# Kernel tuning notes

Measured on AMD Instinct MI355X. Metric: run time of the kernel, lower is better.

## Reference

```python
import jax, jax.numpy as jnp
import numpy as np

B, S, D, H = 2, 2048, 1024, 16
DK = D // H


def setup_inputs() -> dict:
    key = jax.random.key(0)
    ks = jax.random.split(key, 12)
    scale = 1.0 / np.sqrt(D)
    inp = {
        "Q": jax.random.normal(ks[0], (B, S, D), jnp.float32),
        "K": jax.random.normal(ks[1], (B, S, D), jnp.float32),
        "V": jax.random.normal(ks[2], (B, S, D), jnp.float32),
        # causal mask, broadcastable to [B, H, S, S]; 0 -> masked
        "Mask": jnp.tril(jnp.ones((S, S), jnp.int32))[None, None],
        "Wq": jax.random.normal(ks[3], (D, D), jnp.float32) * scale,
        "bq": jnp.zeros((D,), jnp.float32),
        "Wk": jax.random.normal(ks[4], (D, D), jnp.float32) * scale,
        "bk": jnp.zeros((D,), jnp.float32),
        "Wv": jax.random.normal(ks[5], (D, D), jnp.float32) * scale,
        "bv": jnp.zeros((D,), jnp.float32),
        "Wo": jax.random.normal(ks[6], (D, D), jnp.float32) * scale,
        "bo": jnp.zeros((D,), jnp.float32),
    }
    return inp


def _heads(x):
    # [B, S, D] -> [B, H, S, DK]
    return x.reshape(B, S, H, DK).transpose(0, 2, 1, 3)


def reference(Q, K, V, Mask, Wq, bq, Wk, bk, Wv, bv, Wo, bo):
    q = _heads(Q @ Wq.T + bq)
    k = _heads(K @ Wk.T + bk)
    v = _heads(V @ Wv.T + bv)
    # NOTE: original module does NOT scale by 1/sqrt(d_k)
    logits = jnp.einsum("bhqd,bhkd->bhqk", q, k)
    logits = jnp.where(Mask == 0, jnp.float32(-1e9), logits)
    attn = jax.nn.softmax(logits, axis=-1)  # dropout p=0.0 -> identity
    ctx = jnp.einsum("bhqk,bhkd->bhqd", attn, v)
    ctx = ctx.transpose(0, 2, 1, 3).reshape(B, S, D)
    return ctx @ Wo.T + bo
```

## Files before the change

### kernel.cpp

```cpp
#include <hip/hip_runtime.h>
#include <hip/hip_bf16.h>

#define B_  2
#define S_  2048
#define D_  1024
#define H_  16
#define DK_ 64
#define M_  (B_ * S_)

typedef __bf16 bf16;
typedef __bf16 bf16x8 __attribute__((ext_vector_type(8)));
typedef __bf16 bf16x4 __attribute__((ext_vector_type(4)));
typedef float  f32x4  __attribute__((ext_vector_type(4)));

#define MFMA16(a, b, c) __builtin_amdgcn_mfma_f32_16x16x32_bf16((a), (b), (c), 0, 0, 0)

__device__ __forceinline__ void gl2lds16(const bf16* g, bf16* l) {
    __builtin_amdgcn_global_load_lds((const __attribute__((address_space(1))) void*)g,
                                     (__attribute__((address_space(3))) void*)l, 16, 0, 0);
}

struct CastArgs { const float* src[7]; bf16* dst[7]; };

__global__ __launch_bounds__(256) void cast_all(CastArgs a) {
    int i = blockIdx.x * 256 + threadIdx.x;
    int seg, off;
    if (i < 3145728) { seg = i >> 20; off = i & 1048575; }
    else { int j = i - 3145728; seg = 3 + (j >> 18); off = j & 262143; }
    float4 v = ((const float4*)a.src[seg])[off];
    bf16x4 o;
    o[0] = (bf16)v.x; o[1] = (bf16)v.y; o[2] = (bf16)v.z; o[3] = (bf16)v.w;
    *(bf16x4*)&a.dst[seg][(size_t)off * 4] = o;
}

struct QkvArgs { const bf16* A[3]; const bf16* W[3]; const float* bias[3]; bf16* out[3]; };

__global__ __launch_bounds__(256, 3) void gemm_qkv(QkvArgs ar) {
    __shared__ char smem[34816];
    bf16* As = (bf16*)smem;
    bf16* Bs = (bf16*)(smem + 16384);
    bf16* Cs = (bf16*)smem;

    const int hid = (blockIdx.z * gridDim.y + blockIdx.y) * gridDim.x + blockIdx.x;
    const int swz = (hid & 7) * 96 + (hid >> 3);
    const int bx = swz & 7, by = (swz >> 3) & 31, z = swz >> 8;

    const bf16* A  = ar.A[z];
    const bf16* Bt = ar.W[z];
    const float* bias = ar.bias[z];
    bf16* Out = ar.out[z];
    const int mode = (z == 2) ? 1 : 0;

    const int t = threadIdx.x, lane = t & 63, w = t >> 6;
    const int lr = lane & 15, lq = lane >> 4;
    const int wm = (w >> 1) * 64, wn = (w & 1) * 64;
    const int n0 = bx * 128, m0 = by * 128;

    const bf16* Ag[4]; const bf16* Bg[4]; bf16* Al[4]; bf16* Bl[4];
#pragma unroll
    for (int i = 0; i < 4; ++i) {
        int c = i * 256 + w * 64 + lane;
        int row = c >> 3, x = (c & 7) ^ (row & 7);
        Ag[i] = A  + (size_t)(m0 + row) * 1024 + x * 8;
        Bg[i] = Bt + (size_t)(n0 + row) * 1024 + x * 8;
        Al[i] = As + (i * 256 + w * 64) * 8;
        Bl[i] = Bs + (i * 256 + w * 64) * 8;
    }

    f32x4 acc[4][4];
#pragma unroll
    for (int mi = 0; mi < 4; ++mi)
#pragma unroll
        for (int ni = 0; ni < 4; ++ni) acc[mi][ni] = 0.0f;

    for (int k0 = 0; k0 < 1024; k0 += 64) {
        __syncthreads();
#pragma unroll
        for (int i = 0; i < 4; ++i) {
            gl2lds16(Ag[i] + k0, Al[i]);
            gl2lds16(Bg[i] + k0, Bl[i]);
        }
        __syncthreads();
#pragma unroll
        for (int ks = 0; ks < 2; ++ks) {
            bf16x8 af[4], bfr[4];
#pragma unroll
            for (int mi = 0; mi < 4; ++mi) {
                int row = wm + mi * 16 + lr;
                af[mi] = *(const bf16x8*)&As[row * 64 + ((ks * 4 + lq) ^ (row & 7)) * 8];
            }
#pragma unroll
            for (int ni = 0; ni < 4; ++ni) {
                int row = wn + ni * 16 + lr;
                bfr[ni] = *(const bf16x8*)&Bs[row * 64 + ((ks * 4 + lq) ^ (row & 7)) * 8];
            }
#pragma unroll
            for (int mi = 0; mi < 4; ++mi)
#pragma unroll
                for (int ni = 0; ni < 4; ++ni) acc[mi][ni] = MFMA16(af[mi], bfr[ni], acc[mi][ni]);
        }
    }

    if (mode == 0) {
#pragma unroll
        for (int mi = 0; mi < 4; ++mi) {
#pragma unroll
            for (int ni = 0; ni < 4; ++ni) {
                int gn = n0 + wn + ni * 16 + lr;
                float bv = bias[gn];
#pragma unroll
                for (int r = 0; r < 4; ++r) {
                    int gm = m0 + wm + mi * 16 + lq * 4 + r;
                    float v = acc[mi][ni][r] + bv;
                    int b = gm >> 11, s = gm & (S_ - 1);
                    int h = gn >> 6, dk = gn & 63;
                    Out[(((size_t)(b * H_ + h) * S_ + s) << 6) + dk] = (bf16)v;
                }
            }
        }
    } else {
        __syncthreads();
#pragma unroll
        for (int mi = 0; mi < 4; ++mi) {
#pragma unroll
            for (int ni = 0; ni < 4; ++ni) {
                int n = wn + ni * 16 + lr;
                float bv = bias[n0 + n];
                bf16x4 pk;
#pragma unroll
                for (int r = 0; r < 4; ++r) pk[r] = (bf16)(acc[mi][ni][r] + bv);
                *(bf16x4*)&Cs[n * 136 + wm + mi * 16 + lq * 4] = pk;
            }
        }
        __syncthreads();
        const int b = m0 >> 11, s0 = m0 & (S_ - 1);
#pragma unroll
        for (int j = 0; j < 8; ++j) {
            int cc = j * 256 + t;
            int n = cc >> 4, cm = cc & 15;
            int gn = n0 + n, h = gn >> 6, dk = gn & 63;
            bf16x8 v = *(const bf16x8*)&Cs[n * 136 + cm * 8];
            *(bf16x8*)&Out[(((size_t)(b * H_ + h) * DK_ + dk) << 11) + s0 + cm * 8] = v;
        }
    }
}

__global__ __launch_bounds__(256, 2) void gemm_out(const bf16* __restrict__ A,
                                                   const bf16* __restrict__ Bt,
                                                   const float* __restrict__ bias,
                                                   float* __restrict__ Out) {
    __shared__ bf16 As[64 * 64];
    __shared__ bf16 Bs[128 * 64];

    const int hid = blockIdx.y * gridDim.x + blockIdx.x;
    const int swz = (hid & 7) * 64 + (hid >> 3);
    const int bx = swz & 7, by = swz >> 3;

    const int t = threadIdx.x, lane = t & 63, w = t >> 6;
    const int lr = lane & 15, lq = lane >> 4;
    const int wm = (w >> 1) * 32, wn = (w & 1) * 64;
    const int n0 = bx * 128, m0 = by * 64;

    const bf16* Ag[2]; bf16* Al[2];
#pragma unroll
    for (int i = 0; i < 2; ++i) {
        int c = i * 256 + w * 64 + lane;
        int row = c >> 3, x = (c & 7) ^ (row & 7);
        Ag[i] = A + (size_t)(m0 + row) * 1024 + x * 8;
        Al[i] = As + (i * 256 + w * 64) * 8;
    }
    const bf16* Bg[4]; bf16* Bl[4];
#pragma unroll
    for (int i = 0; i < 4; ++i) {
        int c = i * 256 + w * 64 + lane;
        int row = c >> 3, x = (c & 7) ^ (row & 7);
        Bg[i] = Bt + (size_t)(n0 + row) * 1024 + x * 8;
        Bl[i] = Bs + (i * 256 + w * 64) * 8;
    }

    f32x4 acc[2][4];
#pragma unroll
    for (int mi = 0; mi < 2; ++mi)
#pragma unroll
        for (int ni = 0; ni < 4; ++ni) acc[mi][ni] = 0.0f;

    for (int k0 = 0; k0 < 1024; k0 += 64) {
        __syncthreads();
#pragma unroll
        for (int i = 0; i < 2; ++i) gl2lds16(Ag[i] + k0, Al[i]);
#pragma unroll
        for (int i = 0; i < 4; ++i) gl2lds16(Bg[i] + k0, Bl[i]);
        __syncthreads();
#pragma unroll
        for (int ks = 0; ks < 2; ++ks) {
            bf16x8 af[2], bfr[4];
#pragma unroll
            for (int mi = 0; mi < 2; ++mi) {
                int row = wm + mi * 16 + lr;
                af[mi] = *(const bf16x8*)&As[row * 64 + ((ks * 4 + lq) ^ (row & 7)) * 8];
            }
#pragma unroll
            for (int ni = 0; ni < 4; ++ni) {
                int row = wn + ni * 16 + lr;
                bfr[ni] = *(const bf16x8*)&Bs[row * 64 + ((ks * 4 + lq) ^ (row & 7)) * 8];
            }
#pragma unroll
            for (int mi = 0; mi < 2; ++mi)
#pragma unroll
                for (int ni = 0; ni < 4; ++ni) acc[mi][ni] = MFMA16(af[mi], bfr[ni], acc[mi][ni]);
        }
    }

#pragma unroll
    for (int mi = 0; mi < 2; ++mi) {
#pragma unroll
        for (int ni = 0; ni < 4; ++ni) {
            int gn = n0 + wn + ni * 16 + lr;
            float bv = bias[gn];
#pragma unroll
            for (int r = 0; r < 4; ++r) {
                int gm = m0 + wm + mi * 16 + lq * 4 + r;
                Out[(size_t)gm * 1024 + gn] = acc[mi][ni][r] + bv;
            }
        }
    }
}

__global__ __launch_bounds__(256, 2) void flash_attn(const bf16* __restrict__ qh,
                                                     const bf16* __restrict__ kh,
                                                     const bf16* __restrict__ vt,
                                                     bf16* __restrict__ ctx) {
    __shared__ char smem[33280];
    bf16* Ks = (bf16*)smem;
    bf16* Ps = (bf16*)(smem + 16384);
    float* Op = (float*)(smem + 16384);
    float* Lh = (float*)(smem + 32768);

    const int id = blockIdx.x;
    const int xcd = id & 7, loc = id >> 3;
    const int bh = xcd * 4 + (loc & 3);
    const int pair = loc >> 2;
    const int b = bh >> 4, h = bh & 15;

    const bf16* Qp = qh + (size_t)bh * S_ * DK_;
    const bf16* Kp = kh + (size_t)bh * S_ * DK_;
    const bf16* Vp = vt + (size_t)bh * DK_ * S_;

    const int t = threadIdx.x, lane = t & 63, w = t >> 6;
    const int lr = lane & 15, lq = lane >> 4;
    const int wq = w & 1, wk = w >> 1;
    bf16* Pw = Ps + w * 2048;

    for (int half = 0; half < 2; ++half) {
        const int qt = half ? (31 - pair) : pair;

        bf16x8 qreg[2][2];
#pragma unroll
        for (int ks = 0; ks < 2; ++ks)
#pragma unroll
            for (int nt = 0; nt < 2; ++nt)
                qreg[ks][nt] = *(const bf16x8*)(Qp +
                    (size_t)(qt * 64 + wq * 32 + nt * 16 + lr) * 64 + ks * 32 + lq * 8);

        f32x4 oacc[2][4];
#pragma unroll
        for (int mt = 0; mt < 2; ++mt)
#pragma unroll
            for (int nt = 0; nt < 4; ++nt) oacc[mt][nt] = 0.0f;
        float lpart[2] = {0.f, 0.f};

        const int nkt = qt / 2 + 1;
        for (int kt = 0; kt < nkt; ++kt) {
            __syncthreads();
#pragma unroll
            for (int i = 0; i < 4; ++i) {
                int c = w * 256 + i * 64 + lane;
                int krow = c >> 3, xx = (c & 7) ^ (krow & 7);
                gl2lds16(Kp + (size_t)(kt * 128 + krow) * 64 + xx * 8, Ks + (w * 256 + i * 64) * 8);
            }
            __syncthreads();

            const int k64 = kt * 2 + wk;
            if (k64 <= qt) {
                bf16x8 bv[2][4];
#pragma unroll
                for (int kk = 0; kk < 2; ++kk)
#pragma unroll
                    for (int nt = 0; nt < 4; ++nt)
                        bv[kk][nt] = *(const bf16x8*)(Vp + (size_t)(nt * 16 + lr) * S_ +
                                                      kt * 128 + wk * 64 + kk * 32 + lq * 8);
                f32x4 s[4][2];
#pragma unroll
                for (int mt = 0; mt < 4; ++mt)
#pragma unroll
                    for (int nt = 0; nt < 2; ++nt) s[mt][nt] = 0.0f;
#pragma unroll
                for (int ks = 0; ks < 2; ++ks) {
                    bf16x8 af[4];
                    int xx = (ks * 4 + lq) ^ (lr & 7);
#pragma unroll
                    for (int mt = 0; mt < 4; ++mt)
                        af[mt] = *(const bf16x8*)&Ks[(wk * 64 + mt * 16 + lr) * 64 + xx * 8];
#pragma unroll
                    for (int mt = 0; mt < 4; ++mt)
#pragma unroll
                        for (int nt = 0; nt < 2; ++nt) s[mt][nt] = MFMA16(af[mt], qreg[ks][nt], s[mt][nt]);
                }
                const bool diag = (k64 == qt);
#pragma unroll
                for (int mt = 0; mt < 4; ++mt)
#pragma unroll
                    for (int nt = 0; nt < 2; ++nt) {
                        bf16x4 pb;
#pragma unroll
                        for (int r = 0; r < 4; ++r) {
                            int kl = mt * 16 + lq * 4 + r;
                            int qlT = wq * 32 + nt * 16 + lr;
                            float p = (!diag || kl <= qlT) ? __expf(s[mt][nt][r]) : 0.0f;
                            bf16 p16 = (bf16)p;
                            lpart[nt] += (float)p16;
                            pb[r] = p16;
                        }
                        int xx = (2 * mt + (lq >> 1)) ^ (lr & 7);
                        *(bf16x4*)&Pw[(nt * 16 + lr) * 64 + xx * 8 + (lq & 1) * 4] = pb;
                    }
#pragma unroll
                for (int kk = 0; kk < 2; ++kk) {
                    bf16x8 ap[2];
                    int xx = (kk * 4 + lq) ^ (lr & 7);
#pragma unroll
                    for (int mt2 = 0; mt2 < 2; ++mt2)
                        ap[mt2] = *(const bf16x8*)&Pw[(mt2 * 16 + lr) * 64 + xx * 8];
#pragma unroll
                    for (int mt2 = 0; mt2 < 2; ++mt2)
#pragma unroll
                        for (int nt = 0; nt < 4; ++nt)
                            oacc[mt2][nt] = MFMA16(ap[mt2], bv[kk][nt], oacc[mt2][nt]);
                }
            }
        }

        __syncthreads();
#pragma unroll
        for (int nt = 0; nt < 2; ++nt) {
            lpart[nt] += __shfl_xor(lpart[nt], 16);
            lpart[nt] += __shfl_xor(lpart[nt], 32);
        }
        if (lq == 0)
#pragma unroll
            for (int nt = 0; nt < 2; ++nt) Lh[wk * 64 + wq * 32 + nt * 16 + lr] = lpart[nt];
        if (wk == 1) {
#pragma unroll
            for (int mt = 0; mt < 2; ++mt)
#pragma unroll
                for (int nt = 0; nt < 4; ++nt)
#pragma unroll
                    for (int r = 0; r < 4; ++r) {
                        int row = mt * 16 + lq * 4 + r, col = nt * 16 + lr;
                        int xx = (col >> 2) ^ (row & 15);
                        Op[wq * 2048 + row * 64 + xx * 4 + (col & 3)] = oacc[mt][nt][r];
                    }
        }
        __syncthreads();
        if (wk == 0) {
            float linv[2][4];
#pragma unroll
            for (int mt = 0; mt < 2; ++mt)
#pragma unroll
                for (int r = 0; r < 4; ++r) {
                    int qq = wq * 32 + mt * 16 + lq * 4 + r;
                    linv[mt][r] = 1.0f / (Lh[qq] + Lh[64 + qq]);
                }
#pragma unroll
            for (int mt = 0; mt < 2; ++mt)
#pragma unroll
                for (int nt = 0; nt < 4; ++nt)
#pragma unroll
                    for (int r = 0; r < 4; ++r) {
                        int row = mt * 16 + lq * 4 + r, col = nt * 16 + lr;
                        int xx = (col >> 2) ^ (row & 15);
                        float v = (oacc[mt][nt][r] + Op[wq * 2048 + row * 64 + xx * 4 + (col & 3)]) * linv[mt][r];
                        int q = qt * 64 + wq * 32 + row;
                        ctx[((size_t)(b * S_ + q)) * D_ + h * DK_ + col] = (bf16)v;
                    }
        }
        __syncthreads();
    }
}

extern "C" void kernel_launch(void* const* d_in, const int* in_sizes, int n_in,
                              void* d_out, int out_size, void* d_ws, size_t ws_size,
                              hipStream_t stream) {
    const float* Q  = (const float*)d_in[0];
    const float* K  = (const float*)d_in[1];
    const float* V  = (const float*)d_in[2];
    const float* Wq = (const float*)d_in[4];
    const float* bq = (const float*)d_in[5];
    const float* Wk = (const float*)d_in[6];
    const float* bk = (const float*)d_in[7];
    const float* Wv = (const float*)d_in[8];
    const float* bv = (const float*)d_in[9];
    const float* Wo = (const float*)d_in[10];
    const float* bo = (const float*)d_in[11];

    char* p = (char*)d_ws;
    bf16* Qb  = (bf16*)p;  p += (size_t)M_ * D_ * 2;
    bf16* Kb  = (bf16*)p;  p += (size_t)M_ * D_ * 2;
    bf16* Vb  = (bf16*)p;  p += (size_t)M_ * D_ * 2;
    bf16* Wqb = (bf16*)p;  p += (size_t)D_ * D_ * 2;
    bf16* Wkb = (bf16*)p;  p += (size_t)D_ * D_ * 2;
    bf16* Wvb = (bf16*)p;  p += (size_t)D_ * D_ * 2;
    bf16* Wob = (bf16*)p;  p += (size_t)D_ * D_ * 2;
    bf16* qhd = (bf16*)p;  p += (size_t)M_ * D_ * 2;
    bf16* khd = (bf16*)p;  p += (size_t)M_ * D_ * 2;
    bf16* vtr = (bf16*)p;  p += (size_t)M_ * D_ * 2;
    bf16* ctx = (bf16*)p;  p += (size_t)M_ * D_ * 2;

    CastArgs ca;
    ca.src[0] = Q;  ca.dst[0] = Qb;
    ca.src[1] = K;  ca.dst[1] = Kb;
    ca.src[2] = V;  ca.dst[2] = Vb;
    ca.src[3] = Wq; ca.dst[3] = Wqb;
    ca.src[4] = Wk; ca.dst[4] = Wkb;
    ca.src[5] = Wv; ca.dst[5] = Wvb;
    ca.src[6] = Wo; ca.dst[6] = Wob;
    cast_all<<<16384, 256, 0, stream>>>(ca);

    QkvArgs qa;
    qa.A[0] = Qb;  qa.A[1] = Kb;  qa.A[2] = Vb;
    qa.W[0] = Wqb; qa.W[1] = Wkb; qa.W[2] = Wvb;
    qa.bias[0] = bq; qa.bias[1] = bk; qa.bias[2] = bv;
    qa.out[0] = qhd; qa.out[1] = khd; qa.out[2] = vtr;
    dim3 qgrid(D_ / 128, M_ / 128, 3);
    gemm_qkv<<<qgrid, 256, 0, stream>>>(qa);

    flash_attn<<<512, 256, 0, stream>>>(qhd, khd, vtr, ctx);

    dim3 ogrid(D_ / 128, M_ / 64);
    gemm_out<<<ogrid, 256, 0, stream>>>(ctx, Wob, bo, (float*)d_out);
}
```

Measured before the change: 213.8 us.

## Stage QKV epilogue through LDS, grid-stride cast kernel, raise MFMA wave priority

```diff
diff --git a/kernel.cpp b/kernel.cpp
--- a/kernel.cpp
+++ b/kernel.cpp
@@ -23,14 +23,15 @@
 struct CastArgs { const float* src[7]; bf16* dst[7]; };
 
 __global__ __launch_bounds__(256) void cast_all(CastArgs a) {
-    int i = blockIdx.x * 256 + threadIdx.x;
-    int seg, off;
-    if (i < 3145728) { seg = i >> 20; off = i & 1048575; }
-    else { int j = i - 3145728; seg = 3 + (j >> 18); off = j & 262143; }
-    float4 v = ((const float4*)a.src[seg])[off];
-    bf16x4 o;
-    o[0] = (bf16)v.x; o[1] = (bf16)v.y; o[2] = (bf16)v.z; o[3] = (bf16)v.w;
-    *(bf16x4*)&a.dst[seg][(size_t)off * 4] = o;
+    for (int i = blockIdx.x * 256 + threadIdx.x; i < 4194304; i += 2048 * 256) {
+        int seg, off;
+        if (i < 3145728) { seg = i >> 20; off = i & 1048575; }
+        else { int j = i - 3145728; seg = 3 + (j >> 18); off = j & 262143; }
+        float4 v = ((const float4*)a.src[seg])[off];
+        bf16x4 o;
+        o[0] = (bf16)v.x; o[1] = (bf16)v.y; o[2] = (bf16)v.z; o[3] = (bf16)v.w;
+        *(bf16x4*)&a.dst[seg][(size_t)off * 4] = o;
+    }
 }
 
 struct QkvArgs { const bf16* A[3]; const bf16* W[3]; const float* bias[3]; bf16* out[3]; };
@@ -102,21 +103,28 @@
     }
 
     if (mode == 0) {
+        __syncthreads();
 #pragma unroll
         for (int mi = 0; mi < 4; ++mi) {
 #pragma unroll
             for (int ni = 0; ni < 4; ++ni) {
-                int gn = n0 + wn + ni * 16 + lr;
-                float bv = bias[gn];
-#pragma unroll
-                for (int r = 0; r < 4; ++r) {
-                    int gm = m0 + wm + mi * 16 + lq * 4 + r;
-                    float v = acc[mi][ni][r] + bv;
-                    int b = gm >> 11, s = gm & (S_ - 1);
-                    int h = gn >> 6, dk = gn & 63;
-                    Out[(((size_t)(b * H_ + h) * S_ + s) << 6) + dk] = (bf16)v;
-                }
-            }
+                int n = wn + ni * 16 + lr;
+                float bv = bias[n0 + n];
+#pragma unroll
+                for (int r = 0; r < 4; ++r)
+                    Cs[(wm + mi * 16 + lq * 4 + r) * 136 + n] = (bf16)(acc[mi][ni][r] + bv);
+            }
+        }
+        __syncthreads();
+        const int bb = m0 >> 11;
+#pragma unroll
+        for (int j = 0; j < 8; ++j) {
+            int cc = j * 256 + t;
+            int mrow = cc >> 4, c8 = cc & 15;
+            int gn = n0 + c8 * 8, h = gn >> 6, dk = gn & 63;
+            int s = (m0 + mrow) & (S_ - 1);
+            bf16x8 v = *(const bf16x8*)&Cs[mrow * 136 + c8 * 8];
+            *(bf16x8*)&Out[(((size_t)(bb * H_ + h) * S_ + s) << 6) + dk] = v;
         }
     } else {
         __syncthreads();
@@ -294,6 +302,7 @@
                 for (int mt = 0; mt < 4; ++mt)
 #pragma unroll
                     for (int nt = 0; nt < 2; ++nt) s[mt][nt] = 0.0f;
+                __builtin_amdgcn_s_setprio(1);
 #pragma unroll
                 for (int ks = 0; ks < 2; ++ks) {
                     bf16x8 af[4];
@@ -306,6 +315,7 @@
 #pragma unroll
                         for (int nt = 0; nt < 2; ++nt) s[mt][nt] = MFMA16(af[mt], qreg[ks][nt], s[mt][nt]);
                 }
+                __builtin_amdgcn_s_setprio(0);
                 const bool diag = (k64 == qt);
 #pragma unroll
                 for (int mt = 0; mt < 4; ++mt)
@@ -324,6 +334,7 @@
                         int xx = (2 * mt + (lq >> 1)) ^ (lr & 7);
                         *(bf16x4*)&Pw[(nt * 16 + lr) * 64 + xx * 8 + (lq & 1) * 4] = pb;
                     }
+                __builtin_amdgcn_s_setprio(1);
 #pragma unroll
                 for (int kk = 0; kk < 2; ++kk) {
                     bf16x8 ap[2];
@@ -337,6 +348,7 @@
                         for (int nt = 0; nt < 4; ++nt)
                             oacc[mt2][nt] = MFMA16(ap[mt2], bv[kk][nt], oacc[mt2][nt]);
                 }
+                __builtin_amdgcn_s_setprio(0);
             }
         }
 
@@ -424,7 +436,7 @@
     ca.src[4] = Wk; ca.dst[4] = Wkb;
     ca.src[5] = Wv; ca.dst[5] = Wvb;
     ca.src[6] = Wo; ca.dst[6] = Wob;
-    cast_all<<<16384, 256, 0, stream>>>(ca);
+    cast_all<<<2048, 256, 0, stream>>>(ca);
 
     QkvArgs qa;
     qa.A[0] = Qb;  qa.A[1] = Kb;  qa.A[2] = Vb;
```

Measured after the change: 222.0 us. +3.8%, slower.
